# Optimization experiments

Measured on AMD Instinct MI355X. Metric: run time of the kernel, lower is better.

## Reference

```python
import jax, jax.numpy as jnp
import numpy as np

N_NODES = 50000
N_EDGES = 600000
DIM = 128
N_HEADS = 3
EDGE_VOCAB = 22754
NEG_SLOPE = 0.2


def setup_inputs() -> dict:
    key = jax.random.key(0)
    ks = jax.random.split(key, 12)
    s = 1.0 / np.sqrt(DIM)
    return {
        "x": jax.random.normal(ks[0], (N_NODES, DIM), dtype=jnp.float32),
        "edge_index": jax.random.randint(ks[1], (2, N_EDGES), 0, N_NODES, dtype=jnp.int64),
        "edge_ids": jax.random.randint(ks[2], (N_EDGES,), 0, EDGE_VOCAB, dtype=jnp.int64),
        "ddi_weight": jax.random.uniform(ks[3], (N_EDGES,), dtype=jnp.float32),
        "W_lin": jax.random.normal(ks[4], (DIM, DIM), dtype=jnp.float32) * s,
        "b_lin": jnp.zeros((DIM,), dtype=jnp.float32),
        "edge_emb": jax.random.normal(ks[5], (EDGE_VOCAB, 1), dtype=jnp.float32) * 0.1,
        "W_heads": jax.random.normal(ks[6], (N_HEADS, DIM, DIM), dtype=jnp.float32) * s,
        "att_src": jax.random.normal(ks[7], (N_HEADS, DIM), dtype=jnp.float32) * s,
        "att_dst": jax.random.normal(ks[8], (N_HEADS, DIM), dtype=jnp.float32) * s,
        "bias_heads": jnp.zeros((N_HEADS, DIM), dtype=jnp.float32),
    }


def _gat_head(x, src, dst, ew, W, a_src, a_dst, bias):
    # x: [N, D] (already passed through shared lin), ew: [E] scalar edge weights
    h = x @ W                                   # [N, D]
    e = jax.nn.leaky_relu(
        (h @ a_src)[src] + (h @ a_dst)[dst], NEG_SLOPE)   # [E]
    # segment softmax over destination nodes
    e_max = jax.ops.segment_max(e, dst, num_segments=N_NODES)   # [N]
    e_exp = jnp.exp(e - e_max[dst])                              # [E]
    denom = jax.ops.segment_sum(e_exp, dst, num_segments=N_NODES)
    alpha = e_exp / jnp.maximum(denom[dst], 1e-16)               # [E]
    msg = (alpha * ew)[:, None] * h[src]                         # [E, D]
    return jax.ops.segment_sum(msg, dst, num_segments=N_NODES) + bias


def reference(x, edge_index, edge_ids, ddi_weight, W_lin, b_lin, edge_emb,
              W_heads, att_src, att_dst, bias_heads):
    x = x @ W_lin + b_lin                         # shared linear projection
    ew = edge_emb[edge_ids, 0] - ddi_weight        # [E]
    src, dst = edge_index[0], edge_index[1]
    out = jnp.zeros_like(x)
    for hix in range(N_HEADS):                     # small fixed head count
        out = out + _gat_head(x, src, dst, ew, W_heads[hix],
                              att_src[hix], att_dst[hix], bias_heads[hix])
    return out / N_HEADS
```

## Files before the change

kernel.cpp:

```cpp
#include <hip/hip_runtime.h>
#include <math.h>

#define NN 50000
#define NE 600000
#define D 128
#define NH 3
#define CAP 64
#define EDGE_BLOCKS ((NE + 255) / 256)

typedef short bf16x8 __attribute__((ext_vector_type(8)));
typedef float f32x4 __attribute__((ext_vector_type(4)));

__device__ __forceinline__ unsigned short f2b(float f) {
  unsigned int u = __float_as_uint(f);
  u += 0x7FFF + ((u >> 16) & 1);
  return (unsigned short)(u >> 16);
}
__device__ __forceinline__ float blo(unsigned int u) {
  return __uint_as_float(u << 16);
}
__device__ __forceinline__ float bhi(unsigned int u) {
  return __uint_as_float(u & 0xffff0000u);
}

__global__ __launch_bounds__(256) void pack_scatter(const float* __restrict__ W_lin,
                                                    const float* __restrict__ W_heads,
                                                    const float* __restrict__ att_src,
                                                    const float* __restrict__ att_dst,
                                                    const float* __restrict__ b_lin,
                                                    const int* __restrict__ ei,
                                                    const int* __restrict__ eid,
                                                    const float* __restrict__ ddi,
                                                    const float* __restrict__ emb,
                                                    uint4* __restrict__ Bpack,
                                                    float* __restrict__ bcomb,
                                                    float* __restrict__ sbuf,
                                                    int* __restrict__ counts,
                                                    unsigned int* __restrict__ slots8) {
  const int bx = blockIdx.x;
  const int tid = threadIdx.x;
  if (bx < 24) {
    int u = bx * 256 + tid;
    int h = u >> 11, r = u & 2047;
    int nt = r >> 8, s = (r >> 6) & 3, q = (r >> 4) & 3, n0 = r & 15;
    int kbase = s * 32 + q * 8;
    int n = nt * 16 + n0;
    const float* wl = W_lin + kbase * D;
    const float* wh = W_heads + h * D * D + n;
    float vals[8];
    #pragma unroll
    for (int j = 0; j < 8; ++j) vals[j] = 0.f;
    for (int m = 0; m < D; ++m) {
      float whv = wh[m * D];
      #pragma unroll
      for (int j = 0; j < 8; ++j) vals[j] += wl[j * D + m] * whv;
    }
    unsigned int w[4];
    #pragma unroll
    for (int p = 0; p < 4; ++p)
      w[p] = (unsigned int)f2b(vals[2 * p]) | ((unsigned int)f2b(vals[2 * p + 1]) << 16);
    Bpack[h * 2304 + r] = make_uint4(w[0], w[1], w[2], w[3]);
  } else if (bx < 27) {
    const int h = bx - 24;
    __shared__ float wha_s[128], wha_d[128], scs[128], scd[128];
    {
      int m = tid & 127;
      const float* W = W_heads + h * D * D + m * D;
      const float* a = (tid < 128) ? (att_src + h * D) : (att_dst + h * D);
      float acc = 0.f;
      for (int n = 0; n < D; ++n) acc += W[n] * a[n];
      if (tid < 128) wha_s[m] = acc; else wha_d[m] = acc;
    }
    __syncthreads();
    {
      int k = tid & 127;
      const float* wl = W_lin + k * D;
      const float* wha = (tid < 128) ? wha_s : wha_d;
      float acc = 0.f;
      for (int m = 0; m < D; ++m) acc += wl[m] * wha[m];
      if (tid < 128) scs[k] = acc; else scd[k] = acc;
    }
    __syncthreads();
    if (tid < 2) {
      const float* wha = tid ? wha_d : wha_s;
      float a = 0.f;
      for (int k = 0; k < D; ++k) a += b_lin[k] * wha[k];
      sbuf[h * 2 + tid] = a;
    }
    {
      int s = (tid >> 6) & 3, q = (tid >> 4) & 3, n0 = tid & 15;
      int kbase = s * 32 + q * 8;
      float vals[8];
      #pragma unroll
      for (int j = 0; j < 8; ++j)
        vals[j] = (n0 == 0) ? scs[kbase + j] : ((n0 == 1) ? scd[kbase + j] : 0.f);
      unsigned int w[4];
      #pragma unroll
      for (int p = 0; p < 4; ++p)
        w[p] = (unsigned int)f2b(vals[2 * p]) | ((unsigned int)f2b(vals[2 * p + 1]) << 16);
      Bpack[h * 2304 + 2048 + tid] = make_uint4(w[0], w[1], w[2], w[3]);
    }
  } else if (bx < 29) {
    int t = (bx - 27) * 256 + tid;
    if (t < NH * D) {
      int h = t / D, n = t - h * D;
      float acc = 0.f;
      for (int k = 0; k < D; ++k) acc += b_lin[k] * W_heads[h * D * D + k * D + n];
      bcomb[t] = acc;
    }
  } else {
    int e = (bx - 29) * 256 + tid;
    if (e < NE) {
      int src = ei[e], dst = ei[NE + e];
      int idx = atomicAdd(&counts[dst], 1);
      idx = idx < CAP ? idx : CAP - 1;
      float ew = emb[eid[e]] - ddi[e];
      slots8[dst * CAP + idx] = (unsigned int)src | ((unsigned int)f2b(ew) << 16);
    }
  }
}

__global__ __launch_bounds__(256) void mfma_h3s(const float* __restrict__ x,
                                                const uint4* __restrict__ Bpack,
                                                const float* __restrict__ bcomb,
                                                const float* __restrict__ sbuf,
                                                unsigned short* __restrict__ h3,
                                                float* __restrict__ s_src4,
                                                float* __restrict__ s_dst4) {
  const int head = blockIdx.y;
  const int row0 = blockIdx.x * 64;
  const int tid = threadIdx.x;
  __shared__ __align__(16) unsigned short As[64][136];
  #pragma unroll
  for (int it = 0; it < 8; ++it) {
    int idx = tid + it * 256;
    int m = idx >> 5, k4 = idx & 31;
    int row = row0 + m;
    float4 v = make_float4(0.f, 0.f, 0.f, 0.f);
    if (row < NN) v = ((const float4*)(x + (size_t)row * D))[k4];
    uint2 pk;
    pk.x = (unsigned int)f2b(v.x) | ((unsigned int)f2b(v.y) << 16);
    pk.y = (unsigned int)f2b(v.z) | ((unsigned int)f2b(v.w) << 16);
    *((uint2*)&As[m][k4 * 4]) = pk;
  }
  __syncthreads();
  const int wv = tid >> 6;
  const int lane = tid & 63;
  const int n0 = lane & 15, q = lane >> 4;
  const int boff = q * 16 + n0;
  const bf16x8* Bp = (const bf16x8*)(Bpack + head * 2304);

  bf16x8 a4[4];
  #pragma unroll
  for (int s = 0; s < 4; ++s)
    a4[s] = *(const bf16x8*)&As[wv * 16 + n0][s * 32 + q * 8];

  f32x4 acc[9];
  #pragma unroll
  for (int nt = 0; nt < 9; ++nt) acc[nt] = (f32x4){0.f, 0.f, 0.f, 0.f};

  #pragma unroll
  for (int s = 0; s < 4; ++s) {
    #pragma unroll
    for (int nt = 0; nt < 9; ++nt) {
      bf16x8 b = Bp[(nt * 4 + s) * 64 + boff];
      acc[nt] = __builtin_amdgcn_mfma_f32_16x16x32_bf16(a4[s], b, acc[nt], 0, 0, 0);
    }
  }
  __syncthreads();
  const float* bc = bcomb + head * D;
  #pragma unroll
  for (int nt = 0; nt < 8; ++nt) {
    int col = nt * 16 + n0;
    float bv = bc[col];
    #pragma unroll
    for (int r = 0; r < 4; ++r)
      As[wv * 16 + q * 4 + r][col] = f2b(acc[nt][r] + bv);
  }
  if (n0 < 2) {
    float sb = sbuf[head * 2 + n0];
    float* Sout = n0 ? s_dst4 : s_src4;
    #pragma unroll
    for (int r = 0; r < 4; ++r) {
      int row = row0 + wv * 16 + q * 4 + r;
      if (row < NN) Sout[row * 4 + head] = acc[8][r] + sb;
    }
  }
  __syncthreads();
  #pragma unroll
  for (int i = 0; i < 4; ++i) {
    int idx = tid + i * 256;
    int row = idx >> 4, c16 = idx & 15;
    int grow = row0 + row;
    if (grow < NN)
      *((uint4*)&h3[(size_t)grow * (NH * D) + head * D + c16 * 8]) =
          *((const uint4*)&As[row][c16 * 8]);
  }
}

__global__ __launch_bounds__(64) void gather10(const int* __restrict__ counts,
                                               const unsigned int* __restrict__ slots8,
                                               const float4* __restrict__ s_src4,
                                               const float4* __restrict__ s_dst4,
                                               const unsigned short* __restrict__ h3,
                                               const float* __restrict__ bias_heads,
                                               float* __restrict__ out) {
  const int dst = blockIdx.x;
  const int lane = threadIdx.x;
  const int half = lane >> 5;
  const int c = (lane & 31) * 4;
  int cnt = counts[dst];
  cnt = cnt < CAP ? cnt : CAP;
  const int beg = dst * CAP;
  const int end = beg + cnt;
  float4 sd = s_dst4[dst];
  float a0[4] = {0.f, 0.f, 0.f, 0.f};
  float a1[4] = {0.f, 0.f, 0.f, 0.f};
  float a2[4] = {0.f, 0.f, 0.f, 0.f};
  float d0 = 0.f, d1 = 0.f, d2 = 0.f;
  int s = beg + half;
  for (; s + 2 < end; s += 4) {
    unsigned int seA = slots8[s];
    unsigned int seB = slots8[s + 2];
    int srcA = seA & 0xffffu, srcB = seB & 0xffffu;
    float ewA = bhi(seA), ewB = bhi(seB);
    float4 ssA = s_src4[srcA];
    float4 ssB = s_src4[srcB];
    const unsigned short* ha = h3 + (size_t)srcA * (NH * D);
    const unsigned short* hb = h3 + (size_t)srcB * (NH * D);
    uint2 ua0 = *(const uint2*)&ha[c];
    uint2 ua1 = *(const uint2*)&ha[D + c];
    uint2 ua2 = *(const uint2*)&ha[2 * D + c];
    uint2 ub0 = *(const uint2*)&hb[c];
    uint2 ub1 = *(const uint2*)&hb[D + c];
    uint2 ub2 = *(const uint2*)&hb[2 * D + c];
    float vA0 = ssA.x + sd.x, vA1 = ssA.y + sd.y, vA2 = ssA.z + sd.z;
    float vB0 = ssB.x + sd.x, vB1 = ssB.y + sd.y, vB2 = ssB.z + sd.z;
    vA0 = vA0 > 0.f ? vA0 : 0.2f * vA0;
    vA1 = vA1 > 0.f ? vA1 : 0.2f * vA1;
    vA2 = vA2 > 0.f ? vA2 : 0.2f * vA2;
    vB0 = vB0 > 0.f ? vB0 : 0.2f * vB0;
    vB1 = vB1 > 0.f ? vB1 : 0.2f * vB1;
    vB2 = vB2 > 0.f ? vB2 : 0.2f * vB2;
    float pA0 = __expf(vA0), pA1 = __expf(vA1), pA2 = __expf(vA2);
    float pB0 = __expf(vB0), pB1 = __expf(vB1), pB2 = __expf(vB2);
    float wa0 = pA0 * ewA, wa1 = pA1 * ewA, wa2 = pA2 * ewA;
    float wb0 = pB0 * ewB, wb1 = pB1 * ewB, wb2 = pB2 * ewB;
    a0[0] += wa0 * blo(ua0.x) + wb0 * blo(ub0.x);
    a0[1] += wa0 * bhi(ua0.x) + wb0 * bhi(ub0.x);
    a0[2] += wa0 * blo(ua0.y) + wb0 * blo(ub0.y);
    a0[3] += wa0 * bhi(ua0.y) + wb0 * bhi(ub0.y);
    a1[0] += wa1 * blo(ua1.x) + wb1 * blo(ub1.x);
    a1[1] += wa1 * bhi(ua1.x) + wb1 * bhi(ub1.x);
    a1[2] += wa1 * blo(ua1.y) + wb1 * blo(ub1.y);
    a1[3] += wa1 * bhi(ua1.y) + wb1 * bhi(ub1.y);
    a2[0] += wa2 * blo(ua2.x) + wb2 * blo(ub2.x);
    a2[1] += wa2 * bhi(ua2.x) + wb2 * bhi(ub2.x);
    a2[2] += wa2 * blo(ua2.y) + wb2 * blo(ub2.y);
    a2[3] += wa2 * bhi(ua2.y) + wb2 * bhi(ub2.y);
    d0 += pA0 + pB0;
    d1 += pA1 + pB1;
    d2 += pA2 + pB2;
  }
  if (s < end) {
    unsigned int seA = slots8[s];
    int srcA = seA & 0xffffu;
    float ewA = bhi(seA);
    float4 ssA = s_src4[srcA];
    const unsigned short* hp = h3 + (size_t)srcA * (NH * D);
    uint2 u0 = *(const uint2*)&hp[c];
    uint2 u1 = *(const uint2*)&hp[D + c];
    uint2 u2 = *(const uint2*)&hp[2 * D + c];
    float vA0 = ssA.x + sd.x, vA1 = ssA.y + sd.y, vA2 = ssA.z + sd.z;
    vA0 = vA0 > 0.f ? vA0 : 0.2f * vA0;
    vA1 = vA1 > 0.f ? vA1 : 0.2f * vA1;
    vA2 = vA2 > 0.f ? vA2 : 0.2f * vA2;
    float pA0 = __expf(vA0), pA1 = __expf(vA1), pA2 = __expf(vA2);
    float w0 = pA0 * ewA, w1 = pA1 * ewA, w2 = pA2 * ewA;
    a0[0] += w0 * blo(u0.x); a0[1] += w0 * bhi(u0.x);
    a0[2] += w0 * blo(u0.y); a0[3] += w0 * bhi(u0.y);
    a1[0] += w1 * blo(u1.x); a1[1] += w1 * bhi(u1.x);
    a1[2] += w1 * blo(u1.y); a1[3] += w1 * bhi(u1.y);
    a2[0] += w2 * blo(u2.x); a2[1] += w2 * bhi(u2.x);
    a2[2] += w2 * blo(u2.y); a2[3] += w2 * bhi(u2.y);
    d0 += pA0; d1 += pA1; d2 += pA2;
  }
  #pragma unroll
  for (int j = 0; j < 4; ++j) {
    a0[j] += __shfl_xor(a0[j], 32, 64);
    a1[j] += __shfl_xor(a1[j], 32, 64);
    a2[j] += __shfl_xor(a2[j], 32, 64);
  }
  d0 += __shfl_xor(d0, 32, 64);
  d1 += __shfl_xor(d1, 32, 64);
  d2 += __shfl_xor(d2, 32, 64);
  if (half == 0) {
    float r0 = 1.f / fmaxf(d0, 1e-16f);
    float r1 = 1.f / fmaxf(d1, 1e-16f);
    float r2 = 1.f / fmaxf(d2, 1e-16f);
    float4 b0 = ((const float4*)bias_heads)[lane & 31];
    float4 b1 = ((const float4*)bias_heads)[32 + (lane & 31)];
    float4 b2 = ((const float4*)bias_heads)[64 + (lane & 31)];
    float4 o;
    o.x = (a0[0] * r0 + a1[0] * r1 + a2[0] * r2 + b0.x + b1.x + b2.x) * (1.f / 3.f);
    o.y = (a0[1] * r0 + a1[1] * r1 + a2[1] * r2 + b0.y + b1.y + b2.y) * (1.f / 3.f);
    o.z = (a0[2] * r0 + a1[2] * r1 + a2[2] * r2 + b0.z + b1.z + b2.z) * (1.f / 3.f);
    o.w = (a0[3] * r0 + a1[3] * r1 + a2[3] * r2 + b0.w + b1.w + b2.w) * (1.f / 3.f);
    *((float4*)&out[(size_t)dst * D + c]) = o;
  }
}

extern "C" void kernel_launch(void* const* d_in, const int* in_sizes, int n_in,
                              void* d_out, int out_size, void* d_ws, size_t ws_size,
                              hipStream_t stream) {
  const float* x          = (const float*)d_in[0];
  const int*   ei         = (const int*)d_in[1];
  const int*   eid        = (const int*)d_in[2];
  const float* ddi        = (const float*)d_in[3];
  const float* W_lin      = (const float*)d_in[4];
  const float* b_lin      = (const float*)d_in[5];
  const float* emb        = (const float*)d_in[6];
  const float* W_heads    = (const float*)d_in[7];
  const float* att_src    = (const float*)d_in[8];
  const float* att_dst    = (const float*)d_in[9];
  const float* bias_heads = (const float*)d_in[10];
  float* out = (float*)d_out;

  uint4*  Bpack  = (uint4*)d_ws;
  unsigned short* h3 = (unsigned short*)(Bpack + NH * 2304);
  unsigned int* slots8 = (unsigned int*)(h3 + (size_t)NN * NH * D);
  float*  bcomb  = (float*)(slots8 + (size_t)NN * CAP);
  float*  sbuf   = bcomb + NH * D;
  float*  s_src4 = sbuf + 8;
  float*  s_dst4 = s_src4 + (size_t)NN * 4;
  int*    counts = (int*)(s_dst4 + (size_t)NN * 4);

  hipMemsetAsync(counts, 0, (size_t)NN * sizeof(int), stream);
  pack_scatter<<<29 + EDGE_BLOCKS, 256, 0, stream>>>(W_lin, W_heads, att_src,
                                                     att_dst, b_lin, ei, eid, ddi,
                                                     emb, Bpack, bcomb, sbuf,
                                                     counts, slots8);
  mfma_h3s<<<dim3((NN + 63) / 64, NH), 256, 0, stream>>>(x, Bpack, bcomb, sbuf,
                                                         h3, s_src4, s_dst4);
  gather10<<<NN, 64, 0, stream>>>(counts, slots8, (const float4*)s_src4,
                                  (const float4*)s_dst4, h3, bias_heads, out);
}
```

Before: 231.8 us.

## Fuse MFMA projection with edge scatter and zero counts in prep kernel

Replaces the memset and separate scatter/MFMA kernels with a prep kernel that builds weights and zeroes counts, followed by one fused kernel. In that kernel every fourth block runs the bf16 MFMA projection for all three heads, and the remaining blocks do the atomic edge bucketing. Each block now loads and converts x once and reuses it across the three heads instead of once per head. This removes a memset and a kernel launch and lets compute-bound and atomic-bound work overlap, but it lowers the number of GEMM blocks and serialises the three heads inside each block.

New measurement: 328.9 us. +41.9%, slower.

```diff
diff --git a/kernel.cpp b/kernel.cpp
--- a/kernel.cpp
+++ b/kernel.cpp
@@ -7,6 +7,9 @@
 #define NH 3
 #define CAP 64
 #define EDGE_BLOCKS ((NE + 255) / 256)
+#define MFMA_BLOCKS ((NN + 63) / 64)
+#define FUSED_BLOCKS (MFMA_BLOCKS + EDGE_BLOCKS)
+#define ZERO_BLOCKS (((NN / 4) + 255) / 256)
 
 typedef short bf16x8 __attribute__((ext_vector_type(8)));
 typedef float f32x4 __attribute__((ext_vector_type(4)));
@@ -23,20 +26,15 @@
   return __uint_as_float(u & 0xffff0000u);
 }
 
-__global__ __launch_bounds__(256) void pack_scatter(const float* __restrict__ W_lin,
-                                                    const float* __restrict__ W_heads,
-                                                    const float* __restrict__ att_src,
-                                                    const float* __restrict__ att_dst,
-                                                    const float* __restrict__ b_lin,
-                                                    const int* __restrict__ ei,
-                                                    const int* __restrict__ eid,
-                                                    const float* __restrict__ ddi,
-                                                    const float* __restrict__ emb,
-                                                    uint4* __restrict__ Bpack,
-                                                    float* __restrict__ bcomb,
-                                                    float* __restrict__ sbuf,
-                                                    int* __restrict__ counts,
-                                                    unsigned int* __restrict__ slots8) {
+__global__ __launch_bounds__(256) void prep(const float* __restrict__ W_lin,
+                                            const float* __restrict__ W_heads,
+                                            const float* __restrict__ att_src,
+                                            const float* __restrict__ att_dst,
+                                            const float* __restrict__ b_lin,
+                                            uint4* __restrict__ Bpack,
+                                            float* __restrict__ bcomb,
+                                            float* __restrict__ sbuf,
+                                            int* __restrict__ counts) {
   const int bx = blockIdx.x;
   const int tid = threadIdx.x;
   if (bx < 24) {
@@ -109,7 +107,99 @@
       bcomb[t] = acc;
     }
   } else {
-    int e = (bx - 29) * 256 + tid;
+    int idx = (bx - 29) * 256 + tid;
+    if (idx < NN / 4) ((int4*)counts)[idx] = make_int4(0, 0, 0, 0);
+  }
+}
+
+__global__ __launch_bounds__(256) void fused(const float* __restrict__ x,
+                                             const uint4* __restrict__ Bpack,
+                                             const float* __restrict__ bcomb,
+                                             const float* __restrict__ sbuf,
+                                             unsigned short* __restrict__ h3,
+                                             float* __restrict__ s_src4,
+                                             float* __restrict__ s_dst4,
+                                             const int* __restrict__ ei,
+                                             const int* __restrict__ eid,
+                                             const float* __restrict__ ddi,
+                                             const float* __restrict__ emb,
+                                             int* __restrict__ counts,
+                                             unsigned int* __restrict__ slots8) {
+  const int bx = blockIdx.x;
+  const int tid = threadIdx.x;
+  __shared__ __align__(16) unsigned short As[64][136];
+  if ((bx & 3) == 0) {
+    const int row0 = (bx >> 2) * 64;
+    #pragma unroll
+    for (int it = 0; it < 8; ++it) {
+      int idx = tid + it * 256;
+      int m = idx >> 5, k4 = idx & 31;
+      int row = row0 + m;
+      float4 v = make_float4(0.f, 0.f, 0.f, 0.f);
+      if (row < NN) v = ((const float4*)(x + (size_t)row * D))[k4];
+      uint2 pk;
+      pk.x = (unsigned int)f2b(v.x) | ((unsigned int)f2b(v.y) << 16);
+      pk.y = (unsigned int)f2b(v.z) | ((unsigned int)f2b(v.w) << 16);
+      *((uint2*)&As[m][k4 * 4]) = pk;
+    }
+    __syncthreads();
+    const int wv = tid >> 6;
+    const int lane = tid & 63;
+    const int n0 = lane & 15, q = lane >> 4;
+    const int boff = q * 16 + n0;
+
+    bf16x8 a4[4];
+    #pragma unroll
+    for (int s = 0; s < 4; ++s)
+      a4[s] = *(const bf16x8*)&As[wv * 16 + n0][s * 32 + q * 8];
+    __syncthreads();
+
+    for (int head = 0; head < NH; ++head) {
+      const bf16x8* Bp = (const bf16x8*)(Bpack + head * 2304);
+      f32x4 acc[9];
+      #pragma unroll
+      for (int nt = 0; nt < 9; ++nt) acc[nt] = (f32x4){0.f, 0.f, 0.f, 0.f};
+      #pragma unroll
+      for (int s = 0; s < 4; ++s) {
+        #pragma unroll
+        for (int nt = 0; nt < 9; ++nt) {
+          bf16x8 b = Bp[(nt * 4 + s) * 64 + boff];
+          acc[nt] = __builtin_amdgcn_mfma_f32_16x16x32_bf16(a4[s], b, acc[nt], 0, 0, 0);
+        }
+      }
+      if (head) __syncthreads();
+      const float* bc = bcomb + head * D;
+      #pragma unroll
+      for (int nt = 0; nt < 8; ++nt) {
+        int col = nt * 16 + n0;
+        float bv = bc[col];
+        #pragma unroll
+        for (int r = 0; r < 4; ++r)
+          As[wv * 16 + q * 4 + r][col] = f2b(acc[nt][r] + bv);
+      }
+      if (n0 < 2) {
+        float sb = sbuf[head * 2 + n0];
+        float* Sout = n0 ? s_dst4 : s_src4;
+        #pragma unroll
+        for (int r = 0; r < 4; ++r) {
+          int row = row0 + wv * 16 + q * 4 + r;
+          if (row < NN) Sout[row * 4 + head] = acc[8][r] + sb;
+        }
+      }
+      __syncthreads();
+      #pragma unroll
+      for (int i = 0; i < 4; ++i) {
+        int idx = tid + i * 256;
+        int row = idx >> 4, c16 = idx & 15;
+        int grow = row0 + row;
+        if (grow < NN)
+          *((uint4*)&h3[(size_t)grow * (NH * D) + head * D + c16 * 8]) =
+              *((const uint4*)&As[row][c16 * 8]);
+      }
+    }
+  } else {
+    int sb = (bx >> 2) * 3 + (bx & 3) - 1;
+    int e = sb * 256 + tid;
     if (e < NE) {
       int src = ei[e], dst = ei[NE + e];
       int idx = atomicAdd(&counts[dst], 1);
@@ -117,84 +207,6 @@
       float ew = emb[eid[e]] - ddi[e];
       slots8[dst * CAP + idx] = (unsigned int)src | ((unsigned int)f2b(ew) << 16);
     }
-  }
-}
-
-__global__ __launch_bounds__(256) void mfma_h3s(const float* __restrict__ x,
-                                                const uint4* __restrict__ Bpack,
-                                                const float* __restrict__ bcomb,
-                                                const float* __restrict__ sbuf,
-                                                unsigned short* __restrict__ h3,
-                                                float* __restrict__ s_src4,
-                                                float* __restrict__ s_dst4) {
-  const int head = blockIdx.y;
-  const int row0 = blockIdx.x * 64;
-  const int tid = threadIdx.x;
-  __shared__ __align__(16) unsigned short As[64][136];
-  #pragma unroll
-  for (int it = 0; it < 8; ++it) {
-    int idx = tid + it * 256;
-    int m = idx >> 5, k4 = idx & 31;
-    int row = row0 + m;
-    float4 v = make_float4(0.f, 0.f, 0.f, 0.f);
-    if (row < NN) v = ((const float4*)(x + (size_t)row * D))[k4];
-    uint2 pk;
-    pk.x = (unsigned int)f2b(v.x) | ((unsigned int)f2b(v.y) << 16);
-    pk.y = (unsigned int)f2b(v.z) | ((unsigned int)f2b(v.w) << 16);
-    *((uint2*)&As[m][k4 * 4]) = pk;
-  }
-  __syncthreads();
-  const int wv = tid >> 6;
-  const int lane = tid & 63;
-  const int n0 = lane & 15, q = lane >> 4;
-  const int boff = q * 16 + n0;
-  const bf16x8* Bp = (const bf16x8*)(Bpack + head * 2304);
-
-  bf16x8 a4[4];
-  #pragma unroll
-  for (int s = 0; s < 4; ++s)
-    a4[s] = *(const bf16x8*)&As[wv * 16 + n0][s * 32 + q * 8];
-
-  f32x4 acc[9];
-  #pragma unroll
-  for (int nt = 0; nt < 9; ++nt) acc[nt] = (f32x4){0.f, 0.f, 0.f, 0.f};
-
-  #pragma unroll
-  for (int s = 0; s < 4; ++s) {
-    #pragma unroll
-    for (int nt = 0; nt < 9; ++nt) {
-      bf16x8 b = Bp[(nt * 4 + s) * 64 + boff];
-      acc[nt] = __builtin_amdgcn_mfma_f32_16x16x32_bf16(a4[s], b, acc[nt], 0, 0, 0);
-    }
-  }
-  __syncthreads();
-  const float* bc = bcomb + head * D;
-  #pragma unroll
-  for (int nt = 0; nt < 8; ++nt) {
-    int col = nt * 16 + n0;
-    float bv = bc[col];
-    #pragma unroll
-    for (int r = 0; r < 4; ++r)
-      As[wv * 16 + q * 4 + r][col] = f2b(acc[nt][r] + bv);
-  }
-  if (n0 < 2) {
-    float sb = sbuf[head * 2 + n0];
-    float* Sout = n0 ? s_dst4 : s_src4;
-    #pragma unroll
-    for (int r = 0; r < 4; ++r) {
-      int row = row0 + wv * 16 + q * 4 + r;
-      if (row < NN) Sout[row * 4 + head] = acc[8][r] + sb;
-    }
-  }
-  __syncthreads();
-  #pragma unroll
-  for (int i = 0; i < 4; ++i) {
-    int idx = tid + i * 256;
-    int row = idx >> 4, c16 = idx & 15;
-    int grow = row0 + row;
-    if (grow < NN)
-      *((uint4*)&h3[(size_t)grow * (NH * D) + head * D + c16 * 8]) =
-          *((const uint4*)&As[row][c16 * 8]);
   }
 }
 
@@ -335,13 +347,11 @@
   float*  s_dst4 = s_src4 + (size_t)NN * 4;
   int*    counts = (int*)(s_dst4 + (size_t)NN * 4);
 
-  hipMemsetAsync(counts, 0, (size_t)NN * sizeof(int), stream);
-  pack_scatter<<<29 + EDGE_BLOCKS, 256, 0, stream>>>(W_lin, W_heads, att_src,
-                                                     att_dst, b_lin, ei, eid, ddi,
-                                                     emb, Bpack, bcomb, sbuf,
-                                                     counts, slots8);
-  mfma_h3s<<<dim3((NN + 63) / 64, NH), 256, 0, stream>>>(x, Bpack, bcomb, sbuf,
-                                                         h3, s_src4, s_dst4);
+  prep<<<29 + ZERO_BLOCKS, 256, 0, stream>>>(W_lin, W_heads, att_src, att_dst,
+                                             b_lin, Bpack, bcomb, sbuf, counts);
+  fused<<<FUSED_BLOCKS, 256, 0, stream>>>(x, Bpack, bcomb, sbuf, h3, s_src4,
+                                          s_dst4, ei, eid, ddi, emb, counts,
+                                          slots8);
   gather10<<<NN, 64, 0, stream>>>(counts, slots8, (const float4*)s_src4,
                                   (const float4*)s_dst4, h3, bias_heads, out);
 }
```

## Aggregate projected x per head then apply head weights in a final GEMM

Applied to the files above, without the earlier changes.

Reorders the math so the gather aggregates the shared-projected features (128 wide) once per edge instead of three per-head projected rows (384 wide). The per-head weight matrices are then applied after aggregation in a new final MFMA GEMM, which uses a split hi/lo bf16 representation of fp16 aggregates to keep precision. This cuts gather memory traffic per edge roughly threefold. In exchange it adds an extra kernel and an intermediate fp16 buffer of N×3×128 that has to be written and read back.

After: 234.3 us. Within noise of the previous version (+1.1%).

```diff
diff --git a/kernel.cpp b/kernel.cpp
--- a/kernel.cpp
+++ b/kernel.cpp
@@ -7,6 +7,7 @@
 #define NH 3
 #define CAP 64
 #define EDGE_BLOCKS ((NE + 255) / 256)
+#define MFMA_BLOCKS ((NN + 63) / 64)
 
 typedef short bf16x8 __attribute__((ext_vector_type(8)));
 typedef float f32x4 __attribute__((ext_vector_type(4)));
@@ -22,50 +23,82 @@
 __device__ __forceinline__ float bhi(unsigned int u) {
   return __uint_as_float(u & 0xffff0000u);
 }
-
-__global__ __launch_bounds__(256) void pack_scatter(const float* __restrict__ W_lin,
-                                                    const float* __restrict__ W_heads,
-                                                    const float* __restrict__ att_src,
-                                                    const float* __restrict__ att_dst,
-                                                    const float* __restrict__ b_lin,
-                                                    const int* __restrict__ ei,
-                                                    const int* __restrict__ eid,
-                                                    const float* __restrict__ ddi,
-                                                    const float* __restrict__ emb,
-                                                    uint4* __restrict__ Bpack,
-                                                    float* __restrict__ bcomb,
-                                                    float* __restrict__ sbuf,
-                                                    int* __restrict__ counts,
-                                                    unsigned int* __restrict__ slots8) {
+__device__ __forceinline__ float b2f(unsigned short us) {
+  return __uint_as_float((unsigned int)us << 16);
+}
+__device__ __forceinline__ unsigned short f2h(float f) {
+  _Float16 t = (_Float16)f;
+  return *(unsigned short*)&t;
+}
+__device__ __forceinline__ float h2f(unsigned short us) {
+  _Float16 t = *(_Float16*)&us;
+  return (float)t;
+}
+
+__global__ __launch_bounds__(256) void pack_scatter2(const float* __restrict__ W_lin,
+                                                     const float* __restrict__ W_heads,
+                                                     const float* __restrict__ att_src,
+                                                     const float* __restrict__ att_dst,
+                                                     const float* __restrict__ b_lin,
+                                                     const float* __restrict__ bias_heads,
+                                                     const int* __restrict__ ei,
+                                                     const int* __restrict__ eid,
+                                                     const float* __restrict__ ddi,
+                                                     const float* __restrict__ emb,
+                                                     uint4* __restrict__ Bpack,
+                                                     uint4* __restrict__ Wpack3,
+                                                     float* __restrict__ sbuf,
+                                                     float* __restrict__ bcomb2,
+                                                     int* __restrict__ counts,
+                                                     unsigned int* __restrict__ slots8) {
   const int bx = blockIdx.x;
   const int tid = threadIdx.x;
-  if (bx < 24) {
-    int u = bx * 256 + tid;
+  if (bx < EDGE_BLOCKS) {
+    int e = bx * 256 + tid;
+    if (e < NE) {
+      int src = ei[e], dst = ei[NE + e];
+      int idx = atomicAdd(&counts[dst], 1);
+      idx = idx < CAP ? idx : CAP - 1;
+      float ew = emb[eid[e]] - ddi[e];
+      slots8[dst * CAP + idx] = (unsigned int)src | ((unsigned int)f2b(ew) << 16);
+    }
+    return;
+  }
+  const int pb = bx - EDGE_BLOCKS;
+  if (pb < 8) {
+    int r = pb * 256 + tid;
+    int nt = r >> 8, s = (r >> 6) & 3, q = (r >> 4) & 3, n0 = r & 15;
+    int kbase = s * 32 + q * 8;
+    int n = nt * 16 + n0;
+    unsigned int w[4];
+    #pragma unroll
+    for (int p = 0; p < 4; ++p) {
+      unsigned short lo = f2b(W_lin[(kbase + 2 * p) * D + n]);
+      unsigned short hi = f2b(W_lin[(kbase + 2 * p + 1) * D + n]);
+      w[p] = (unsigned int)lo | ((unsigned int)hi << 16);
+    }
+    Bpack[r] = make_uint4(w[0], w[1], w[2], w[3]);
+  } else if (pb < 32) {
+    int u = (pb - 8) * 256 + tid;
     int h = u >> 11, r = u & 2047;
     int nt = r >> 8, s = (r >> 6) & 3, q = (r >> 4) & 3, n0 = r & 15;
     int kbase = s * 32 + q * 8;
     int n = nt * 16 + n0;
-    const float* wl = W_lin + kbase * D;
-    const float* wh = W_heads + h * D * D + n;
-    float vals[8];
-    #pragma unroll
-    for (int j = 0; j < 8; ++j) vals[j] = 0.f;
-    for (int m = 0; m < D; ++m) {
-      float whv = wh[m * D];
-      #pragma unroll
-      for (int j = 0; j < 8; ++j) vals[j] += wl[j * D + m] * whv;
-    }
+    const float* W = W_heads + (size_t)h * D * D;
     unsigned int w[4];
     #pragma unroll
-    for (int p = 0; p < 4; ++p)
-      w[p] = (unsigned int)f2b(vals[2 * p]) | ((unsigned int)f2b(vals[2 * p + 1]) << 16);
-    Bpack[h * 2304 + r] = make_uint4(w[0], w[1], w[2], w[3]);
-  } else if (bx < 27) {
-    const int h = bx - 24;
+    for (int p = 0; p < 4; ++p) {
+      unsigned short lo = f2b(W[(kbase + 2 * p) * D + n]);
+      unsigned short hi = f2b(W[(kbase + 2 * p + 1) * D + n]);
+      w[p] = (unsigned int)lo | ((unsigned int)hi << 16);
+    }
+    Wpack3[h * 2048 + r] = make_uint4(w[0], w[1], w[2], w[3]);
+  } else if (pb < 35) {
+    const int h = pb - 32;
     __shared__ float wha_s[128], wha_d[128], scs[128], scd[128];
     {
       int m = tid & 127;
-      const float* W = W_heads + h * D * D + m * D;
+      const float* W = W_heads + (size_t)h * D * D + m * D;
       const float* a = (tid < 128) ? (att_src + h * D) : (att_dst + h * D);
       float acc = 0.f;
       for (int n = 0; n < D; ++n) acc += W[n] * a[n];
@@ -90,44 +123,33 @@
     {
       int s = (tid >> 6) & 3, q = (tid >> 4) & 3, n0 = tid & 15;
       int kbase = s * 32 + q * 8;
-      float vals[8];
-      #pragma unroll
-      for (int j = 0; j < 8; ++j)
-        vals[j] = (n0 == 0) ? scs[kbase + j] : ((n0 == 1) ? scd[kbase + j] : 0.f);
-      unsigned int w[4];
-      #pragma unroll
-      for (int p = 0; p < 4; ++p)
-        w[p] = (unsigned int)f2b(vals[2 * p]) | ((unsigned int)f2b(vals[2 * p + 1]) << 16);
-      Bpack[h * 2304 + 2048 + tid] = make_uint4(w[0], w[1], w[2], w[3]);
-    }
-  } else if (bx < 29) {
-    int t = (bx - 27) * 256 + tid;
-    if (t < NH * D) {
-      int h = t / D, n = t - h * D;
-      float acc = 0.f;
-      for (int k = 0; k < D; ++k) acc += b_lin[k] * W_heads[h * D * D + k * D + n];
-      bcomb[t] = acc;
+      bool mine = (n0 < 6) && ((n0 >> 1) == h);
+      bool zero = (h == 0) && (n0 >= 6);
+      if (mine || zero) {
+        float vals[8];
+        #pragma unroll
+        for (int j = 0; j < 8; ++j)
+          vals[j] = zero ? 0.f : ((n0 & 1) ? scd[kbase + j] : scs[kbase + j]);
+        unsigned int w[4];
+        #pragma unroll
+        for (int p = 0; p < 4; ++p)
+          w[p] = (unsigned int)f2b(vals[2 * p]) | ((unsigned int)f2b(vals[2 * p + 1]) << 16);
+        Bpack[2048 + tid] = make_uint4(w[0], w[1], w[2], w[3]);
+      }
     }
   } else {
-    int e = (bx - 29) * 256 + tid;
-    if (e < NE) {
-      int src = ei[e], dst = ei[NE + e];
-      int idx = atomicAdd(&counts[dst], 1);
-      idx = idx < CAP ? idx : CAP - 1;
-      float ew = emb[eid[e]] - ddi[e];
-      slots8[dst * CAP + idx] = (unsigned int)src | ((unsigned int)f2b(ew) << 16);
-    }
-  }
-}
-
-__global__ __launch_bounds__(256) void mfma_h3s(const float* __restrict__ x,
-                                                const uint4* __restrict__ Bpack,
-                                                const float* __restrict__ bcomb,
-                                                const float* __restrict__ sbuf,
-                                                unsigned short* __restrict__ h3,
-                                                float* __restrict__ s_src4,
-                                                float* __restrict__ s_dst4) {
-  const int head = blockIdx.y;
+    if (tid < D)
+      bcomb2[tid] = (bias_heads[tid] + bias_heads[D + tid] + bias_heads[2 * D + tid]) * (1.f / 3.f);
+  }
+}
+
+__global__ __launch_bounds__(256) void mfma_x(const float* __restrict__ x,
+                                              const uint4* __restrict__ Bpack,
+                                              const float* __restrict__ b_lin,
+                                              const float* __restrict__ sbuf,
+                                              unsigned short* __restrict__ xb,
+                                              float* __restrict__ s_src4,
+                                              float* __restrict__ s_dst4) {
   const int row0 = blockIdx.x * 64;
   const int tid = threadIdx.x;
   __shared__ __align__(16) unsigned short As[64][136];
@@ -148,7 +170,7 @@
   const int lane = tid & 63;
   const int n0 = lane & 15, q = lane >> 4;
   const int boff = q * 16 + n0;
-  const bf16x8* Bp = (const bf16x8*)(Bpack + head * 2304);
+  const bf16x8* Bp = (const bf16x8*)Bpack;
 
   bf16x8 a4[4];
   #pragma unroll
@@ -168,22 +190,21 @@
     }
   }
   __syncthreads();
-  const float* bc = bcomb + head * D;
   #pragma unroll
   for (int nt = 0; nt < 8; ++nt) {
     int col = nt * 16 + n0;
-    float bv = bc[col];
+    float bv = b_lin[col];
     #pragma unroll
     for (int r = 0; r < 4; ++r)
       As[wv * 16 + q * 4 + r][col] = f2b(acc[nt][r] + bv);
   }
-  if (n0 < 2) {
-    float sb = sbuf[head * 2 + n0];
-    float* Sout = n0 ? s_dst4 : s_src4;
+  if (n0 < 6) {
+    float sb = sbuf[n0];
+    float* Sout = (n0 & 1) ? s_dst4 : s_src4;
     #pragma unroll
     for (int r = 0; r < 4; ++r) {
       int row = row0 + wv * 16 + q * 4 + r;
-      if (row < NN) Sout[row * 4 + head] = acc[8][r] + sb;
+      if (row < NN) Sout[row * 4 + (n0 >> 1)] = acc[8][r] + sb;
     }
   }
   __syncthreads();
@@ -193,21 +214,19 @@
     int row = idx >> 4, c16 = idx & 15;
     int grow = row0 + row;
     if (grow < NN)
-      *((uint4*)&h3[(size_t)grow * (NH * D) + head * D + c16 * 8]) =
-          *((const uint4*)&As[row][c16 * 8]);
-  }
-}
-
-__global__ __launch_bounds__(64) void gather10(const int* __restrict__ counts,
+      *((uint4*)&xb[(size_t)grow * D + c16 * 8]) = *((const uint4*)&As[row][c16 * 8]);
+  }
+}
+
+__global__ __launch_bounds__(64) void gather12(const int* __restrict__ counts,
                                                const unsigned int* __restrict__ slots8,
                                                const float4* __restrict__ s_src4,
                                                const float4* __restrict__ s_dst4,
-                                               const unsigned short* __restrict__ h3,
-                                               const float* __restrict__ bias_heads,
-                                               float* __restrict__ out) {
+                                               const unsigned short* __restrict__ xb,
+                                               unsigned short* __restrict__ accb) {
   const int dst = blockIdx.x;
   const int lane = threadIdx.x;
-  const int half = lane >> 5;
+  const int hf = lane >> 5;
   const int c = (lane & 31) * 4;
   int cnt = counts[dst];
   cnt = cnt < CAP ? cnt : CAP;
@@ -218,7 +237,7 @@
   float a1[4] = {0.f, 0.f, 0.f, 0.f};
   float a2[4] = {0.f, 0.f, 0.f, 0.f};
   float d0 = 0.f, d1 = 0.f, d2 = 0.f;
-  int s = beg + half;
+  int s = beg + hf;
   for (; s + 2 < end; s += 4) {
     unsigned int seA = slots8[s];
     unsigned int seB = slots8[s + 2];
@@ -226,14 +245,8 @@
     float ewA = bhi(seA), ewB = bhi(seB);
     float4 ssA = s_src4[srcA];
     float4 ssB = s_src4[srcB];
-    const unsigned short* ha = h3 + (size_t)srcA * (NH * D);
-    const unsigned short* hb = h3 + (size_t)srcB * (NH * D);
-    uint2 ua0 = *(const uint2*)&ha[c];
-    uint2 ua1 = *(const uint2*)&ha[D + c];
-    uint2 ua2 = *(const uint2*)&ha[2 * D + c];
-    uint2 ub0 = *(const uint2*)&hb[c];
-    uint2 ub1 = *(const uint2*)&hb[D + c];
-    uint2 ub2 = *(const uint2*)&hb[2 * D + c];
+    uint2 ua = *(const uint2*)&xb[(size_t)srcA * D + c];
+    uint2 ub = *(const uint2*)&xb[(size_t)srcB * D + c];
     float vA0 = ssA.x + sd.x, vA1 = ssA.y + sd.y, vA2 = ssA.z + sd.z;
     float vB0 = ssB.x + sd.x, vB1 = ssB.y + sd.y, vB2 = ssB.z + sd.z;
     vA0 = vA0 > 0.f ? vA0 : 0.2f * vA0;
@@ -246,18 +259,14 @@
     float pB0 = __expf(vB0), pB1 = __expf(vB1), pB2 = __expf(vB2);
     float wa0 = pA0 * ewA, wa1 = pA1 * ewA, wa2 = pA2 * ewA;
     float wb0 = pB0 * ewB, wb1 = pB1 * ewB, wb2 = pB2 * ewB;
-    a0[0] += wa0 * blo(ua0.x) + wb0 * blo(ub0.x);
-    a0[1] += wa0 * bhi(ua0.x) + wb0 * bhi(ub0.x);
-    a0[2] += wa0 * blo(ua0.y) + wb0 * blo(ub0.y);
-    a0[3] += wa0 * bhi(ua0.y) + wb0 * bhi(ub0.y);
-    a1[0] += wa1 * blo(ua1.x) + wb1 * blo(ub1.x);
-    a1[1] += wa1 * bhi(ua1.x) + wb1 * bhi(ub1.x);
-    a1[2] += wa1 * blo(ua1.y) + wb1 * blo(ub1.y);
-    a1[3] += wa1 * bhi(ua1.y) + wb1 * bhi(ub1.y);
-    a2[0] += wa2 * blo(ua2.x) + wb2 * blo(ub2.x);
-    a2[1] += wa2 * bhi(ua2.x) + wb2 * bhi(ub2.x);
-    a2[2] += wa2 * blo(ua2.y) + wb2 * blo(ub2.y);
-    a2[3] += wa2 * bhi(ua2.y) + wb2 * bhi(ub2.y);
+    float xA[4] = {blo(ua.x), bhi(ua.x), blo(ua.y), bhi(ua.y)};
+    float xB[4] = {blo(ub.x), bhi(ub.x), blo(ub.y), bhi(ub.y)};
+    #pragma unroll
+    for (int j = 0; j < 4; ++j) {
+      a0[j] += wa0 * xA[j] + wb0 * xB[j];
+      a1[j] += wa1 * xA[j] + wb1 * xB[j];
+      a2[j] += wa2 * xA[j] + wb2 * xB[j];
+    }
     d0 += pA0 + pB0;
     d1 += pA1 + pB1;
     d2 += pA2 + pB2;
@@ -267,22 +276,20 @@
     int srcA = seA & 0xffffu;
     float ewA = bhi(seA);
     float4 ssA = s_src4[srcA];
-    const unsigned short* hp = h3 + (size_t)srcA * (NH * D);
-    uint2 u0 = *(const uint2*)&hp[c];
-    uint2 u1 = *(const uint2*)&hp[D + c];
-    uint2 u2 = *(const uint2*)&hp[2 * D + c];
+    uint2 ua = *(const uint2*)&xb[(size_t)srcA * D + c];
     float vA0 = ssA.x + sd.x, vA1 = ssA.y + sd.y, vA2 = ssA.z + sd.z;
     vA0 = vA0 > 0.f ? vA0 : 0.2f * vA0;
     vA1 = vA1 > 0.f ? vA1 : 0.2f * vA1;
     vA2 = vA2 > 0.f ? vA2 : 0.2f * vA2;
     float pA0 = __expf(vA0), pA1 = __expf(vA1), pA2 = __expf(vA2);
     float w0 = pA0 * ewA, w1 = pA1 * ewA, w2 = pA2 * ewA;
-    a0[0] += w0 * blo(u0.x); a0[1] += w0 * bhi(u0.x);
-    a0[2] += w0 * blo(u0.y); a0[3] += w0 * bhi(u0.y);
-    a1[0] += w1 * blo(u1.x); a1[1] += w1 * bhi(u1.x);
-    a1[2] += w1 * blo(u1.y); a1[3] += w1 * bhi(u1.y);
-    a2[0] += w2 * blo(u2.x); a2[1] += w2 * bhi(u2.x);
-    a2[2] += w2 * blo(u2.y); a2[3] += w2 * bhi(u2.y);
+    float xA[4] = {blo(ua.x), bhi(ua.x), blo(ua.y), bhi(ua.y)};
+    #pragma unroll
+    for (int j = 0; j < 4; ++j) {
+      a0[j] += w0 * xA[j];
+      a1[j] += w1 * xA[j];
+      a2[j] += w2 * xA[j];
+    }
     d0 += pA0; d1 += pA1; d2 += pA2;
   }
   #pragma unroll
@@ -294,19 +301,104 @@
   d0 += __shfl_xor(d0, 32, 64);
   d1 += __shfl_xor(d1, 32, 64);
   d2 += __shfl_xor(d2, 32, 64);
-  if (half == 0) {
-    float r0 = 1.f / fmaxf(d0, 1e-16f);
-    float r1 = 1.f / fmaxf(d1, 1e-16f);
-    float r2 = 1.f / fmaxf(d2, 1e-16f);
-    float4 b0 = ((const float4*)bias_heads)[lane & 31];
-    float4 b1 = ((const float4*)bias_heads)[32 + (lane & 31)];
-    float4 b2 = ((const float4*)bias_heads)[64 + (lane & 31)];
-    float4 o;
-    o.x = (a0[0] * r0 + a1[0] * r1 + a2[0] * r2 + b0.x + b1.x + b2.x) * (1.f / 3.f);
-    o.y = (a0[1] * r0 + a1[1] * r1 + a2[1] * r2 + b0.y + b1.y + b2.y) * (1.f / 3.f);
-    o.z = (a0[2] * r0 + a1[2] * r1 + a2[2] * r2 + b0.z + b1.z + b2.z) * (1.f / 3.f);
-    o.w = (a0[3] * r0 + a1[3] * r1 + a2[3] * r2 + b0.w + b1.w + b2.w) * (1.f / 3.f);
-    *((float4*)&out[(size_t)dst * D + c]) = o;
+  if (hf == 0) {
+    float r0 = 1.f / (3.f * fmaxf(d0, 1e-16f));
+    float r1 = 1.f / (3.f * fmaxf(d1, 1e-16f));
+    float r2 = 1.f / (3.f * fmaxf(d2, 1e-16f));
+    unsigned short* base = accb + (size_t)dst * (NH * D);
+    uint2 o;
+    o.x = (unsigned int)f2h(a0[0] * r0) | ((unsigned int)f2h(a0[1] * r0) << 16);
+    o.y = (unsigned int)f2h(a0[2] * r0) | ((unsigned int)f2h(a0[3] * r0) << 16);
+    *(uint2*)&base[c] = o;
+    o.x = (unsigned int)f2h(a1[0] * r1) | ((unsigned int)f2h(a1[1] * r1) << 16);
+    o.y = (unsigned int)f2h(a1[2] * r1) | ((unsigned int)f2h(a1[3] * r1) << 16);
+    *(uint2*)&base[D + c] = o;
+    o.x = (unsigned int)f2h(a2[0] * r2) | ((unsigned int)f2h(a2[1] * r2) << 16);
+    o.y = (unsigned int)f2h(a2[2] * r2) | ((unsigned int)f2h(a2[3] * r2) << 16);
+    *(uint2*)&base[2 * D + c] = o;
+  }
+}
+
+__global__ __launch_bounds__(256) void final_gemm(const unsigned short* __restrict__ accb,
+                                                  const uint4* __restrict__ Wpack3,
+                                                  const float* __restrict__ bcomb2,
+                                                  float* __restrict__ out) {
+  const int row0 = blockIdx.x * 64;
+  const int tid = threadIdx.x;
+  __shared__ __align__(16) unsigned short Ah[64][136];
+  __shared__ __align__(16) unsigned short Al[64][136];
+  const int wv = tid >> 6;
+  const int lane = tid & 63;
+  const int n0 = lane & 15, q = lane >> 4;
+  const int boff = q * 16 + n0;
+
+  f32x4 o[8];
+  #pragma unroll
+  for (int nt = 0; nt < 8; ++nt) o[nt] = (f32x4){0.f, 0.f, 0.f, 0.f};
+
+  for (int chunk = 0; chunk < NH; ++chunk) {
+    if (chunk) __syncthreads();
+    #pragma unroll
+    for (int it = 0; it < 4; ++it) {
+      int idx = tid + it * 256;
+      int m = idx >> 4, k8 = idx & 15;
+      int row = row0 + m;
+      uint4 u = make_uint4(0, 0, 0, 0);
+      if (row < NN)
+        u = *(const uint4*)&accb[(size_t)row * (NH * D) + chunk * D + k8 * 8];
+      const unsigned int* pu = (const unsigned int*)&u;
+      unsigned int hw[2], lw[2];
+      #pragma unroll
+      for (int p = 0; p < 2; ++p) {
+        unsigned short hh[4], ll[4];
+        #pragma unroll
+        for (int e = 0; e < 2; ++e) {
+          unsigned int word = pu[2 * p + e];
+          float f0 = h2f((unsigned short)(word & 0xffffu));
+          float f1 = h2f((unsigned short)(word >> 16));
+          unsigned short h0 = f2b(f0), h1 = f2b(f1);
+          hh[2 * e] = h0; hh[2 * e + 1] = h1;
+          ll[2 * e] = f2b(f0 - b2f(h0));
+          ll[2 * e + 1] = f2b(f1 - b2f(h1));
+        }
+        hw[p] = (unsigned int)hh[0] | ((unsigned int)hh[1] << 16);
+        lw[p] = (unsigned int)ll[0] | ((unsigned int)ll[1] << 16);
+        hw[p] |= 0; lw[p] |= 0;
+        if (true) {
+          ((unsigned int*)&Ah[m][k8 * 8])[2 * p]     = (unsigned int)hh[0] | ((unsigned int)hh[1] << 16);
+          ((unsigned int*)&Ah[m][k8 * 8])[2 * p + 1] = (unsigned int)hh[2] | ((unsigned int)hh[3] << 16);
+          ((unsigned int*)&Al[m][k8 * 8])[2 * p]     = (unsigned int)ll[0] | ((unsigned int)ll[1] << 16);
+          ((unsigned int*)&Al[m][k8 * 8])[2 * p + 1] = (unsigned int)ll[2] | ((unsigned int)ll[3] << 16);
+        }
+      }
+    }
+    __syncthreads();
+    bf16x8 ah[4], al[4];
+    #pragma unroll
+    for (int s = 0; s < 4; ++s) {
+      ah[s] = *(const bf16x8*)&Ah[wv * 16 + n0][s * 32 + q * 8];
+      al[s] = *(const bf16x8*)&Al[wv * 16 + n0][s * 32 + q * 8];
+    }
+    const bf16x8* Bp = (const bf16x8*)(Wpack3 + chunk * 2048);
+    #pragma unroll
+    for (int s = 0; s < 4; ++s) {
+      #pragma unroll
+      for (int nt = 0; nt < 8; ++nt) {
+        bf16x8 b = Bp[(nt * 4 + s) * 64 + boff];
+        o[nt] = __builtin_amdgcn_mfma_f32_16x16x32_bf16(ah[s], b, o[nt], 0, 0, 0);
+        o[nt] = __builtin_amdgcn_mfma_f32_16x16x32_bf16(al[s], b, o[nt], 0, 0, 0);
+      }
+    }
+  }
+  #pragma unroll
+  for (int nt = 0; nt < 8; ++nt) {
+    int col = nt * 16 + n0;
+    float bv = bcomb2[col];
+    #pragma unroll
+    for (int r = 0; r < 4; ++r) {
+      int row = row0 + wv * 16 + q * 4 + r;
+      if (row < NN) out[(size_t)row * D + col] = o[nt][r] + bv;
+    }
   }
 }
 
@@ -327,21 +419,23 @@
   float* out = (float*)d_out;
 
   uint4*  Bpack  = (uint4*)d_ws;
-  unsigned short* h3 = (unsigned short*)(Bpack + NH * 2304);
-  unsigned int* slots8 = (unsigned int*)(h3 + (size_t)NN * NH * D);
-  float*  bcomb  = (float*)(slots8 + (size_t)NN * CAP);
-  float*  sbuf   = bcomb + NH * D;
-  float*  s_src4 = sbuf + 8;
+  uint4*  Wpack3 = Bpack + 2304;
+  unsigned short* xb = (unsigned short*)(Wpack3 + NH * 2048);
+  unsigned int* slots8 = (unsigned int*)(xb + (size_t)NN * D);
+  unsigned short* accb = (unsigned short*)(slots8 + (size_t)NN * CAP);
+  float*  sbuf   = (float*)(accb + (size_t)NN * NH * D);
+  float*  bcomb2 = sbuf + 8;
+  float*  s_src4 = bcomb2 + 128;
   float*  s_dst4 = s_src4 + (size_t)NN * 4;
   int*    counts = (int*)(s_dst4 + (size_t)NN * 4);
 
   hipMemsetAsync(counts, 0, (size_t)NN * sizeof(int), stream);
-  pack_scatter<<<29 + EDGE_BLOCKS, 256, 0, stream>>>(W_lin, W_heads, att_src,
-                                                     att_dst, b_lin, ei, eid, ddi,
-                                                     emb, Bpack, bcomb, sbuf,
-                                                     counts, slots8);
-  mfma_h3s<<<dim3((NN + 63) / 64, NH), 256, 0, stream>>>(x, Bpack, bcomb, sbuf,
-                                                         h3, s_src4, s_dst4);
-  gather10<<<NN, 64, 0, stream>>>(counts, slots8, (const float4*)s_src4,
-                                  (const float4*)s_dst4, h3, bias_heads, out);
-}
+  pack_scatter2<<<EDGE_BLOCKS + 36, 256, 0, stream>>>(
+      W_lin, W_heads, att_src, att_dst, b_lin, bias_heads, ei, eid, ddi, emb,
+      Bpack, Wpack3, sbuf, bcomb2, counts, slots8);
+  mfma_x<<<MFMA_BLOCKS, 256, 0, stream>>>(x, Bpack, b_lin, sbuf, xb,
+                                          s_src4, s_dst4);
+  gather12<<<NN, 64, 0, stream>>>(counts, slots8, (const float4*)s_src4,
+                                  (const float4*)s_dst4, xb, accb);
+  final_gemm<<<MFMA_BLOCKS, 256, 0, stream>>>(accb, Wpack3, bcomb2, out);
+}
```
